# Performance work log

Measured on AMD Instinct MI355X. Metric: run time of the kernel, lower is better.

Reference implementation:

```python
import jax, jax.numpy as jnp
import numpy as np

SCALING = 32.0 / 8.0  # alpha / rank

def setup_inputs() -> dict:
    key = jax.random.key(0)
    k1, k2, k3, k4, k5 = jax.random.split(key, 5)
    B, S, D_in, D_out, R = 4, 2048, 1600, 4800, 8
    x = jax.random.normal(k1, (B, S, D_in), dtype=jnp.float32)
    W = jax.random.normal(k2, (D_in, D_out), dtype=jnp.float32) * 0.02
    b = jax.random.normal(k3, (D_out,), dtype=jnp.float32) * 0.02
    lora_A = jax.random.normal(k4, (D_in, R), dtype=jnp.float32) * 0.02
    lora_B = jax.random.normal(k5, (R, D_out), dtype=jnp.float32) * 0.02
    return {"x": x, "W": W, "b": b, "lora_A": lora_A, "lora_B": lora_B}

def reference(x, W, b, lora_A, lora_B):
    # base Conv1D: x @ W + b  (GPT-2 Conv1D semantics)
    base = jnp.einsum('bsd,df->bsf', x, W) + b
    # low-rank LoRA path: (x @ A) @ B, scaled
    lora = jnp.einsum('bsr,rf->bsf', jnp.einsum('bsd,dr->bsr', x, lora_A), lora_B)
    return base + lora * SCALING
```

## Files before the change

### kernel.cpp

```cpp
#include <hip/hip_runtime.h>
#include <hip/hip_bf16.h>


#define M_ROWS 8192
#define K_DIM  1600
#define N_DIM  4800
#define KP     1664

#define BM 128
#define BN 160
#define BK 64
#define KT (KP / BK)

#define NXB 1024
#define NWB (75 * 50)
#define NLB 19

typedef __attribute__((ext_vector_type(4))) float f32x4;
typedef __attribute__((ext_vector_type(8))) short s16x8;

static __device__ __forceinline__ unsigned short f2bf(float f) {
    unsigned int u = __float_as_uint(f);
    u += 0x7fffu + ((u >> 16) & 1u);
    return (unsigned short)(u >> 16);
}

typedef __attribute__((address_space(3))) unsigned int as3_uint;
typedef __attribute__((address_space(1))) const unsigned int as1_uint;

static __device__ __forceinline__ void gl16(const unsigned short* g,
                                            unsigned short* l) {
    __builtin_amdgcn_global_load_lds((as1_uint*)g, (as3_uint*)l, 16, 0, 0);
}

__global__ __launch_bounds__(256) void prep_all(const float* __restrict__ x,
                                                const float* __restrict__ W,
                                                const float* __restrict__ lora_A,
                                                const float* __restrict__ lora_B,
                                                unsigned short* __restrict__ Xbp,
                                                unsigned short* __restrict__ Wtp) {
    __shared__ float tile[32][65];
    const int bid = blockIdx.x;
    const int t   = threadIdx.x;

    if (bid < NXB) {
        const int lane = t & 63;
        const int w    = t >> 6;
        const int m0   = bid * 8 + w * 2;
        const float* xr0 = x + (size_t)m0 * K_DIM;
        const float* xr1 = xr0 + K_DIM;
        unsigned short* o0 = Xbp + (size_t)m0 * KP;
        unsigned short* o1 = o0 + KP;

        float a0[8], a1[8];
#pragma unroll
        for (int r = 0; r < 8; ++r) { a0[r] = 0.f; a1[r] = 0.f; }

        for (int g = lane; g < 400; g += 64) {
            const float4* ap = (const float4*)(lora_A + (size_t)32 * g);
            float4 x0 = ((const float4*)xr0)[g];
            float4 x1 = ((const float4*)xr1)[g];

            ushort4 s0, s1;
            s0.x = f2bf(x0.x); s0.y = f2bf(x0.y); s0.z = f2bf(x0.z); s0.w = f2bf(x0.w);
            s1.x = f2bf(x1.x); s1.y = f2bf(x1.y); s1.z = f2bf(x1.z); s1.w = f2bf(x1.w);
            ((ushort4*)o0)[g] = s0;
            ((ushort4*)o1)[g] = s1;

            float xs0[4] = {x0.x, x0.y, x0.z, x0.w};
            float xs1[4] = {x1.x, x1.y, x1.z, x1.w};
#pragma unroll
            for (int j = 0; j < 4; ++j) {
                float4 lo = ap[2 * j + 0];
                float4 hi = ap[2 * j + 1];
                a0[0] += xs0[j] * lo.x; a0[1] += xs0[j] * lo.y;
                a0[2] += xs0[j] * lo.z; a0[3] += xs0[j] * lo.w;
                a0[4] += xs0[j] * hi.x; a0[5] += xs0[j] * hi.y;
                a0[6] += xs0[j] * hi.z; a0[7] += xs0[j] * hi.w;
                a1[0] += xs1[j] * lo.x; a1[1] += xs1[j] * lo.y;
                a1[2] += xs1[j] * lo.z; a1[3] += xs1[j] * lo.w;
                a1[4] += xs1[j] * hi.x; a1[5] += xs1[j] * hi.y;
                a1[6] += xs1[j] * hi.z; a1[7] += xs1[j] * hi.w;
            }
        }

#pragma unroll
        for (int off = 1; off < 64; off <<= 1) {
#pragma unroll
            for (int r = 0; r < 8; ++r) {
                a0[r] += __shfl_xor(a0[r], off, 64);
                a1[r] += __shfl_xor(a1[r], off, 64);
            }
        }

        if (lane < 16) {
            ushort4 t0, t1;
            t0.x = 0; t0.y = 0; t0.z = 0; t0.w = 0;
            t1 = t0;
            if (lane == 0) {
                t0.x = f2bf(a0[0]); t0.y = f2bf(a0[1]); t0.z = f2bf(a0[2]); t0.w = f2bf(a0[3]);
                t1.x = f2bf(a1[0]); t1.y = f2bf(a1[1]); t1.z = f2bf(a1[2]); t1.w = f2bf(a1[3]);
            } else if (lane == 1) {
                t0.x = f2bf(a0[4]); t0.y = f2bf(a0[5]); t0.z = f2bf(a0[6]); t0.w = f2bf(a0[7]);
                t1.x = f2bf(a1[4]); t1.y = f2bf(a1[5]); t1.z = f2bf(a1[6]); t1.w = f2bf(a1[7]);
            }
            ((ushort4*)o0)[400 + lane] = t0;
            ((ushort4*)o1)[400 + lane] = t1;
        }
        return;
    }

    if (bid < NXB + NWB) {
        const int wid = bid - NXB;
        const int n0  = (wid % 75) * 64;
        const int k0  = (wid / 75) * 32;

#pragma unroll
        for (int p = 0; p < 2; ++p) {
            const int k  = p * 16 + (t >> 4);
            const int c4 = (t & 15) * 4;
            float4 v = *(const float4*)(W + (size_t)(k0 + k) * N_DIM + n0 + c4);
            tile[k][c4 + 0] = v.x; tile[k][c4 + 1] = v.y;
            tile[k][c4 + 2] = v.z; tile[k][c4 + 3] = v.w;
        }
        __syncthreads();

        const int n   = t >> 2;
        const int seg = t & 3;
        unsigned int pk[4];
#pragma unroll
        for (int h = 0; h < 4; ++h) {
            unsigned int lo = f2bf(tile[seg * 8 + 2 * h + 0][n]);
            unsigned int hi = f2bf(tile[seg * 8 + 2 * h + 1][n]);
            pk[h] = lo | (hi << 16);
        }
        uint4 o = {pk[0], pk[1], pk[2], pk[3]};
        *(uint4*)(Wtp + (size_t)(n0 + n) * KP + k0 + seg * 8) = o;
        return;
    }

    {
        const int lid = bid - (NXB + NWB);
        const int n = lid * 256 + t;
        if (n >= N_DIM) return;
        ushort4* d4 = (ushort4*)(Wtp + (size_t)n * KP + 1600);
        ushort4 o0, o1, z;
        o0.x = f2bf(4.0f * lora_B[0 * N_DIM + n]);
        o0.y = f2bf(4.0f * lora_B[1 * N_DIM + n]);
        o0.z = f2bf(4.0f * lora_B[2 * N_DIM + n]);
        o0.w = f2bf(4.0f * lora_B[3 * N_DIM + n]);
        o1.x = f2bf(4.0f * lora_B[4 * N_DIM + n]);
        o1.y = f2bf(4.0f * lora_B[5 * N_DIM + n]);
        o1.z = f2bf(4.0f * lora_B[6 * N_DIM + n]);
        o1.w = f2bf(4.0f * lora_B[7 * N_DIM + n]);
        z.x = 0; z.y = 0; z.z = 0; z.w = 0;
        d4[0] = o0;
        d4[1] = o1;
#pragma unroll
        for (int i = 2; i < 16; ++i) d4[i] = z;
    }
}

__global__ __launch_bounds__(256, 3) void gemm_bt(const unsigned short* __restrict__ Ab,
                                                  const unsigned short* __restrict__ Bb,
                                                  const float* __restrict__ bias,
                                                  float* __restrict__ out) {
    __shared__ unsigned short lsA[BM * BK];
    __shared__ unsigned short lsB[BN * BK];

    const int t    = threadIdx.x;
    const int n0   = blockIdx.x * BN;
    const int m0   = blockIdx.y * BM;
    const int lane = t & 63;
    const int w    = t >> 6;
    const int wr   = (w >> 1) * 64;
    const int wc   = (w & 1) * 80;
    const int lr   = lane & 15;
    const int quad = lane >> 4;

    const int rS = lane >> 3;
    const int gS = ((lane & 7) ^ (rS & 7)) * 8;
    const unsigned short* srcA = Ab + (size_t)(m0 + rS) * KP + gS;
    const unsigned short* srcB = Bb + (size_t)(n0 + rS) * KP + gS;

    int rowA[4], rowB[5];
#pragma unroll
    for (int mt = 0; mt < 4; ++mt) rowA[mt] = (wr + mt * 16 + lr) * BK;
#pragma unroll
    for (int nt = 0; nt < 5; ++nt) rowB[nt] = (wc + nt * 16 + lr) * BK;
    const int lx = lr & 7;

    f32x4 acc[4][5];
#pragma unroll
    for (int mt = 0; mt < 4; ++mt)
#pragma unroll
        for (int nt = 0; nt < 5; ++nt) acc[mt][nt] = (f32x4)0.f;

    for (int kt = 0; kt < KT; ++kt) {
        const int kb = kt * BK;
        __syncthreads();
#pragma unroll
        for (int c = w; c < 16; c += 4)
            gl16(srcA + (size_t)c * 8 * KP + kb, &lsA[c * 512]);
#pragma unroll
        for (int c = w; c < 20; c += 4)
            gl16(srcB + (size_t)c * 8 * KP + kb, &lsB[c * 512]);
        __syncthreads();

#pragma unroll
        for (int ksub = 0; ksub < 2; ++ksub) {
            const int g0 = quad + ksub * 4;
            const int koff = ((g0 ^ lx)) * 8;
            s16x8 af[4], bf[5];
#pragma unroll
            for (int mt = 0; mt < 4; ++mt) af[mt] = *(const s16x8*)&lsA[rowA[mt] + koff];
#pragma unroll
            for (int nt = 0; nt < 5; ++nt) bf[nt] = *(const s16x8*)&lsB[rowB[nt] + koff];
#pragma unroll
            for (int mt = 0; mt < 4; ++mt)
#pragma unroll
                for (int nt = 0; nt < 5; ++nt)
                    acc[mt][nt] = __builtin_amdgcn_mfma_f32_16x16x32_bf16(
                        af[mt], bf[nt], acc[mt][nt], 0, 0, 0);
        }
    }

#pragma unroll
    for (int nt = 0; nt < 5; ++nt) {
        const int gc = n0 + wc + nt * 16 + lr;
        const float bv = bias[gc];
#pragma unroll
        for (int mt = 0; mt < 4; ++mt) {
#pragma unroll
            for (int r = 0; r < 4; ++r) {
                const int grow = m0 + wr + mt * 16 + quad * 4 + r;
                out[(size_t)grow * N_DIM + gc] = acc[mt][nt][r] + bv;
            }
        }
    }
}

extern "C" void kernel_launch(void* const* d_in, const int* in_sizes, int n_in,
                              void* d_out, int out_size, void* d_ws, size_t ws_size,
                              hipStream_t stream) {
    const float* x      = (const float*)d_in[0];
    const float* W      = (const float*)d_in[1];
    const float* b      = (const float*)d_in[2];
    const float* lora_A = (const float*)d_in[3];
    const float* lora_B = (const float*)d_in[4];
    float* out = (float*)d_out;

    unsigned short* Xbp = (unsigned short*)d_ws;
    unsigned short* Wtp = Xbp + (size_t)M_ROWS * KP;

    prep_all<<<NXB + NWB + NLB, 256, 0, stream>>>(x, W, lora_A, lora_B, Xbp, Wtp);
    gemm_bt<<<dim3(N_DIM / BN, M_ROWS / BM), 256, 0, stream>>>(Xbp, Wtp, b, out);
}
```

Baseline: 383.8 us.

## Triple-buffer LDS with async prefetch, enlarge tile to 256x160, swizzle blocks

Replaces the load-then-compute loop, which needed two barriers per k-step, with a three-stage LDS ring. Tiles are prefetched two steps ahead, and per-wave s_waitcnt vmcnt counts let global loads overlap the MFMA work behind a single barrier. The M tile grows to 256 rows with 512 threads, and a 1D grid with a block swizzle groups nearby tiles for L2 reuse. MFMA sections also get a raised s_setprio. The ring uses about 156KB of LDS, so only one block fits per CU. The 960 blocks then run as a partial final wave, which may leave some CUs idle.

```diff
diff --git a/kernel.cpp b/kernel.cpp
--- a/kernel.cpp
+++ b/kernel.cpp
@@ -7,7 +7,7 @@
 #define N_DIM  4800
 #define KP     1664
 
-#define BM 128
+#define BM 256
 #define BN 160
 #define BK 64
 #define KT (KP / BK)
@@ -161,34 +161,39 @@
     }
 }
 
-__global__ __launch_bounds__(256, 3) void gemm_bt(const unsigned short* __restrict__ Ab,
+__global__ __launch_bounds__(512, 2) void gemm_bt(const unsigned short* __restrict__ Ab,
                                                   const unsigned short* __restrict__ Bb,
                                                   const float* __restrict__ bias,
                                                   float* __restrict__ out) {
-    __shared__ unsigned short lsA[BM * BK];
-    __shared__ unsigned short lsB[BN * BK];
+    __shared__ unsigned short lsA[3][BM * BK];
+    __shared__ unsigned short lsB[3][BN * BK];
 
     const int t    = threadIdx.x;
-    const int n0   = blockIdx.x * BN;
-    const int m0   = blockIdx.y * BM;
     const int lane = t & 63;
     const int w    = t >> 6;
+
+    const int orig = blockIdx.x;
+    const int swz  = (orig & 7) * 120 + (orig >> 3);
+    const int n0   = (swz % 30) * BN;
+    const int m0   = (swz / 30) * BM;
+
     const int wr   = (w >> 1) * 64;
     const int wc   = (w & 1) * 80;
     const int lr   = lane & 15;
     const int quad = lane >> 4;
+    const int lx   = lr & 7;
 
     const int rS = lane >> 3;
     const int gS = ((lane & 7) ^ (rS & 7)) * 8;
     const unsigned short* srcA = Ab + (size_t)(m0 + rS) * KP + gS;
     const unsigned short* srcB = Bb + (size_t)(n0 + rS) * KP + gS;
+    const bool wlow = (w < 4);
 
     int rowA[4], rowB[5];
 #pragma unroll
     for (int mt = 0; mt < 4; ++mt) rowA[mt] = (wr + mt * 16 + lr) * BK;
 #pragma unroll
     for (int nt = 0; nt < 5; ++nt) rowB[nt] = (wc + nt * 16 + lr) * BK;
-    const int lx = lr & 7;
 
     f32x4 acc[4][5];
 #pragma unroll
@@ -196,34 +201,62 @@
 #pragma unroll
         for (int nt = 0; nt < 5; ++nt) acc[mt][nt] = (f32x4)0.f;
 
+#define STAGE(ktile, buf)                                                     \
+    do {                                                                      \
+        const int kb_ = (ktile) * BK;                                         \
+        _Pragma("unroll")                                                     \
+        for (int c = w; c < 32; c += 8)                                       \
+            gl16(srcA + (size_t)c * 8 * KP + kb_, &lsA[(buf)][c * 512]);      \
+        _Pragma("unroll")                                                     \
+        for (int c = w; c < 20; c += 8)                                       \
+            gl16(srcB + (size_t)c * 8 * KP + kb_, &lsB[(buf)][c * 512]);      \
+    } while (0)
+
+    STAGE(0, 0);
+    STAGE(1, 1);
+    if (wlow) asm volatile("s_waitcnt vmcnt(7)" ::: "memory");
+    else      asm volatile("s_waitcnt vmcnt(6)" ::: "memory");
+    __builtin_amdgcn_sched_barrier(0);
+    __builtin_amdgcn_s_barrier();
+
+    int cb = 0, sb = 2;
     for (int kt = 0; kt < KT; ++kt) {
-        const int kb = kt * BK;
-        __syncthreads();
-#pragma unroll
-        for (int c = w; c < 16; c += 4)
-            gl16(srcA + (size_t)c * 8 * KP + kb, &lsA[c * 512]);
-#pragma unroll
-        for (int c = w; c < 20; c += 4)
-            gl16(srcB + (size_t)c * 8 * KP + kb, &lsB[c * 512]);
-        __syncthreads();
-
+        if (kt + 2 < KT) STAGE(kt + 2, sb);
+
+        const unsigned short* bA = &lsA[cb][0];
+        const unsigned short* bB = &lsB[cb][0];
 #pragma unroll
         for (int ksub = 0; ksub < 2; ++ksub) {
             const int g0 = quad + ksub * 4;
-            const int koff = ((g0 ^ lx)) * 8;
+            const int koff = (g0 ^ lx) * 8;
             s16x8 af[4], bf[5];
 #pragma unroll
-            for (int mt = 0; mt < 4; ++mt) af[mt] = *(const s16x8*)&lsA[rowA[mt] + koff];
-#pragma unroll
-            for (int nt = 0; nt < 5; ++nt) bf[nt] = *(const s16x8*)&lsB[rowB[nt] + koff];
+            for (int mt = 0; mt < 4; ++mt) af[mt] = *(const s16x8*)&bA[rowA[mt] + koff];
+#pragma unroll
+            for (int nt = 0; nt < 5; ++nt) bf[nt] = *(const s16x8*)&bB[rowB[nt] + koff];
+            __builtin_amdgcn_s_setprio(1);
 #pragma unroll
             for (int mt = 0; mt < 4; ++mt)
 #pragma unroll
                 for (int nt = 0; nt < 5; ++nt)
                     acc[mt][nt] = __builtin_amdgcn_mfma_f32_16x16x32_bf16(
                         af[mt], bf[nt], acc[mt][nt], 0, 0, 0);
-        }
-    }
+            __builtin_amdgcn_s_setprio(0);
+        }
+
+        if (kt < KT - 2) {
+            if (wlow) asm volatile("s_waitcnt vmcnt(7)" ::: "memory");
+            else      asm volatile("s_waitcnt vmcnt(6)" ::: "memory");
+        } else {
+            asm volatile("s_waitcnt vmcnt(0)" ::: "memory");
+        }
+        __builtin_amdgcn_sched_barrier(0);
+        __builtin_amdgcn_s_barrier();
+
+        cb = (cb == 2) ? 0 : cb + 1;
+        sb = (sb == 2) ? 0 : sb + 1;
+    }
+#undef STAGE
 
 #pragma unroll
     for (int nt = 0; nt < 5; ++nt) {
@@ -254,5 +287,5 @@
     unsigned short* Wtp = Xbp + (size_t)M_ROWS * KP;
 
     prep_all<<<NXB + NWB + NLB, 256, 0, stream>>>(x, W, lora_A, lora_B, Xbp, Wtp);
-    gemm_bt<<<dim3(N_DIM / BN, M_ROWS / BM), 256, 0, stream>>>(Xbp, Wtp, b, out);
-}
+    gemm_bt<<<dim3((N_DIM / BN) * (M_ROWS / BM)), 512, 0, stream>>>(Xbp, Wtp, b, out);
+}
```

Result: slower. 424.4 us (+10.6%).

## Double-buffer LDS tiles in GEMM and swizzle block order across XCDs

Applied to the files above, without the earlier changes.

Adds a second LDS buffer for the A and B tiles so the load of the next K tile is issued before the MFMAs on the current tile, which removes one barrier per iteration. The grid becomes 1D with a block-id remap that groups tiles for each XCD, meant to improve L2 reuse. Occupancy hint drops from 3 to 2 blocks because LDS use doubles. The gl16 loads are likely direct-to-LDS with no explicit wait before the barrier, so ordering now depends on the barrier semantics.

```diff
diff --git a/kernel.cpp b/kernel.cpp
--- a/kernel.cpp
+++ b/kernel.cpp
@@ -161,22 +161,27 @@
     }
 }
 
-__global__ __launch_bounds__(256, 3) void gemm_bt(const unsigned short* __restrict__ Ab,
+__global__ __launch_bounds__(256, 2) void gemm_bt(const unsigned short* __restrict__ Ab,
                                                   const unsigned short* __restrict__ Bb,
                                                   const float* __restrict__ bias,
                                                   float* __restrict__ out) {
-    __shared__ unsigned short lsA[BM * BK];
-    __shared__ unsigned short lsB[BN * BK];
+    __shared__ unsigned short lsA[2][BM * BK];
+    __shared__ unsigned short lsB[2][BN * BK];
 
     const int t    = threadIdx.x;
-    const int n0   = blockIdx.x * BN;
-    const int m0   = blockIdx.y * BM;
     const int lane = t & 63;
     const int w    = t >> 6;
+
+    const int bid  = blockIdx.x;
+    const int swz  = (bid & 7) * 240 + (bid >> 3);
+    const int m0   = (swz / 30) * BM;
+    const int n0   = (swz % 30) * BN;
+
     const int wr   = (w >> 1) * 64;
     const int wc   = (w & 1) * 80;
     const int lr   = lane & 15;
     const int quad = lane >> 4;
+    const int lx   = lr & 7;
 
     const int rS = lane >> 3;
     const int gS = ((lane & 7) ^ (rS & 7)) * 8;
@@ -188,7 +193,6 @@
     for (int mt = 0; mt < 4; ++mt) rowA[mt] = (wr + mt * 16 + lr) * BK;
 #pragma unroll
     for (int nt = 0; nt < 5; ++nt) rowB[nt] = (wc + nt * 16 + lr) * BK;
-    const int lx = lr & 7;
 
     f32x4 acc[4][5];
 #pragma unroll
@@ -196,26 +200,35 @@
 #pragma unroll
         for (int nt = 0; nt < 5; ++nt) acc[mt][nt] = (f32x4)0.f;
 
+#define STAGE(ktile, buf)                                                     \
+    do {                                                                      \
+        const int kb_ = (ktile) * BK;                                         \
+        _Pragma("unroll")                                                     \
+        for (int c = w; c < 16; c += 4)                                       \
+            gl16(srcA + (size_t)c * 8 * KP + kb_, &lsA[(buf)][c * 512]);      \
+        _Pragma("unroll")                                                     \
+        for (int c = w; c < 20; c += 4)                                       \
+            gl16(srcB + (size_t)c * 8 * KP + kb_, &lsB[(buf)][c * 512]);      \
+    } while (0)
+
+    STAGE(0, 0);
+    __syncthreads();
+
+    int cur = 0;
     for (int kt = 0; kt < KT; ++kt) {
-        const int kb = kt * BK;
-        __syncthreads();
-#pragma unroll
-        for (int c = w; c < 16; c += 4)
-            gl16(srcA + (size_t)c * 8 * KP + kb, &lsA[c * 512]);
-#pragma unroll
-        for (int c = w; c < 20; c += 4)
-            gl16(srcB + (size_t)c * 8 * KP + kb, &lsB[c * 512]);
-        __syncthreads();
-
+        if (kt + 1 < KT) STAGE(kt + 1, cur ^ 1);
+
+        const unsigned short* bA = &lsA[cur][0];
+        const unsigned short* bB = &lsB[cur][0];
 #pragma unroll
         for (int ksub = 0; ksub < 2; ++ksub) {
             const int g0 = quad + ksub * 4;
-            const int koff = ((g0 ^ lx)) * 8;
+            const int koff = (g0 ^ lx) * 8;
             s16x8 af[4], bf[5];
 #pragma unroll
-            for (int mt = 0; mt < 4; ++mt) af[mt] = *(const s16x8*)&lsA[rowA[mt] + koff];
-#pragma unroll
-            for (int nt = 0; nt < 5; ++nt) bf[nt] = *(const s16x8*)&lsB[rowB[nt] + koff];
+            for (int mt = 0; mt < 4; ++mt) af[mt] = *(const s16x8*)&bA[rowA[mt] + koff];
+#pragma unroll
+            for (int nt = 0; nt < 5; ++nt) bf[nt] = *(const s16x8*)&bB[rowB[nt] + koff];
 #pragma unroll
             for (int mt = 0; mt < 4; ++mt)
 #pragma unroll
@@ -223,7 +236,11 @@
                     acc[mt][nt] = __builtin_amdgcn_mfma_f32_16x16x32_bf16(
                         af[mt], bf[nt], acc[mt][nt], 0, 0, 0);
         }
-    }
+
+        __syncthreads();
+        cur ^= 1;
+    }
+#undef STAGE
 
 #pragma unroll
     for (int nt = 0; nt < 5; ++nt) {
@@ -254,5 +271,5 @@
     unsigned short* Wtp = Xbp + (size_t)M_ROWS * KP;
 
     prep_all<<<NXB + NWB + NLB, 256, 0, stream>>>(x, W, lora_A, lora_B, Xbp, Wtp);
-    gemm_bt<<<dim3(N_DIM / BN, M_ROWS / BM), 256, 0, stream>>>(Xbp, Wtp, b, out);
-}
+    gemm_bt<<<dim3((N_DIM / BN) * (M_ROWS / BM)), 256, 0, stream>>>(Xbp, Wtp, b, out);
+}
```

Result: no change. 387.5 us (+1.0%).
